# Optimization experiments

Hardware: AMD Instinct MI355X
Metric: run time of the kernel (lower is better)

Reference implementation:

```python
import jax, jax.numpy as jnp
import numpy as np

B, N, S, K = 16, 4096, 1024, 32
C_PTS = 64
MLP = [64, 64, 128]
EPS = 1e-5


def setup_inputs() -> dict:
    key = jax.random.key(0)
    ks = jax.random.split(key, 2 + len(MLP))
    inp = {
        "xyz": jax.random.normal(ks[0], (B, N, 3), jnp.float32),
        "points": jax.random.normal(ks[1], (B, N, C_PTS), jnp.float32),
    }
    last = 3 + C_PTS
    for i, o in enumerate(MLP):
        inp[f"w{i}"] = jax.random.normal(ks[2 + i], (o, last), jnp.float32) / np.sqrt(last).astype(np.float32)
        inp[f"b{i}"] = jnp.zeros((o,), jnp.float32)
        inp[f"gamma{i}"] = jnp.ones((o,), jnp.float32)
        inp[f"beta{i}"] = jnp.zeros((o,), jnp.float32)
        last = o
    return inp


def _farthest_point_sample(xyz, n_samples):
    # Sequential FPS; start index 0 (torch version uses a random start).
    b, n, _ = xyz.shape

    def step(carry, _):
        distance, farthest = carry  # [B,N], [B]
        centroid = jnp.take_along_axis(xyz, farthest[:, None, None], axis=1)  # [B,1,3]
        dist = jnp.sum((xyz - centroid) ** 2, axis=-1)  # [B,N]
        distance = jnp.minimum(distance, dist)
        new_far = jnp.argmax(distance, axis=-1).astype(jnp.int32)
        return (distance, new_far), farthest

    init = (jnp.full((b, n), 1e10, xyz.dtype), jnp.zeros((b,), jnp.int32))
    _, idxs = jax.lax.scan(step, init, None, length=n_samples)
    return idxs.T  # [B,S]


def _square_distance(src, dst):
    # ||src||^2 + ||dst||^2 - 2 src.dst  -> [B, S, N]
    return (jnp.sum(src ** 2, -1)[:, :, None]
            + jnp.sum(dst ** 2, -1)[:, None, :]
            - 2.0 * jnp.einsum('bsc,bnc->bsn', src, dst))


_gather = jax.vmap(lambda a, i: a[i])  # per-batch fancy gather


def _mlp_layer(x, w, bias, gamma, beta):
    # x: [B,S,K,Cin]; 1x1 conv == channel matmul, then training-mode BN over (B,S,K), then ReLU.
    y = jnp.einsum('bskc,oc->bsko', x, w) + bias
    mean = jnp.mean(y, axis=(0, 1, 2))
    var = jnp.mean((y - mean) ** 2, axis=(0, 1, 2))
    y = (y - mean) * jax.lax.rsqrt(var + EPS) * gamma + beta
    return jax.nn.relu(y)


def reference(xyz, points, w0, b0, gamma0, beta0, w1, b1, gamma1, beta1, w2, b2, gamma2, beta2):
    fps_idx = _farthest_point_sample(xyz, S)                   # [B,S]
    new_xyz = _gather(xyz, fps_idx)                            # [B,S,3]
    dists = _square_distance(new_xyz, xyz)                     # [B,S,N]
    nn_idx = jax.lax.top_k(-dists, K)[1]                       # [B,S,K]
    grouped_xyz = _gather(xyz, nn_idx)                         # [B,S,K,3]
    grouped_pts = _gather(points, nn_idx)                      # [B,S,K,C]
    feat = jnp.concatenate([grouped_xyz - new_xyz[:, :, None, :], grouped_pts], axis=-1)  # [B,S,K,3+C]
    x = _mlp_layer(feat, w0, b0, gamma0, beta0)
    x = _mlp_layer(x, w1, b1, gamma1, beta1)
    x = _mlp_layer(x, w2, b2, gamma2, beta2)
    new_points = jnp.max(x, axis=2)                            # [B,S,Cout]
    new_points = jnp.transpose(new_points, (0, 2, 1))          # [B,Cout,S] matches torch output
    return new_xyz, new_points
```

## Files before the change

kernel.cpp:

```cpp
#include <hip/hip_runtime.h>

#define B_ 16
#define N_ 4096
#define S_ 1024
#define K_ 32
#define NSLOT 128
#define CNT_F 524288.0f
#define RWS 524288

typedef unsigned short ushort_t;
typedef short short8 __attribute__((ext_vector_type(8)));
typedef float floatx4 __attribute__((ext_vector_type(4)));
union U4S8 { uint4 u; short8 v; };

__device__ __forceinline__ ushort_t f2bf(float f) {
  unsigned u = __float_as_uint(f);
  unsigned r = (u + 0x7fffu + ((u >> 16) & 1u)) >> 16;
  return (ushort_t)r;
}
__device__ __forceinline__ unsigned pkrne(float a, float b) {
  return (unsigned)f2bf(a) | ((unsigned)f2bf(b) << 16);
}
__device__ __forceinline__ unsigned pkhu(float a, float b) {
  return ((__float_as_uint(a) + 0x8000u) >> 16) |
         ((__float_as_uint(b) + 0x8000u) & 0xffff0000u);
}

__device__ __forceinline__ uint4 bn_relu_pack(uint4 xv, float4 sca, float4 scb,
                                              float4 sha, float4 shb) {
  float x0 = __uint_as_float(xv.x << 16);
  float x1 = __uint_as_float(xv.x & 0xffff0000u);
  float x2 = __uint_as_float(xv.y << 16);
  float x3 = __uint_as_float(xv.y & 0xffff0000u);
  float x4 = __uint_as_float(xv.z << 16);
  float x5 = __uint_as_float(xv.z & 0xffff0000u);
  float x6 = __uint_as_float(xv.w << 16);
  float x7 = __uint_as_float(xv.w & 0xffff0000u);
  x0 = fmaxf(fmaf(x0, sca.x, sha.x), 0.0f);
  x1 = fmaxf(fmaf(x1, sca.y, sha.y), 0.0f);
  x2 = fmaxf(fmaf(x2, sca.z, sha.z), 0.0f);
  x3 = fmaxf(fmaf(x3, sca.w, sha.w), 0.0f);
  x4 = fmaxf(fmaf(x4, scb.x, shb.x), 0.0f);
  x5 = fmaxf(fmaf(x5, scb.y, shb.y), 0.0f);
  x6 = fmaxf(fmaf(x6, scb.z, shb.z), 0.0f);
  x7 = fmaxf(fmaf(x7, scb.w, shb.w), 0.0f);
  return make_uint4(pkhu(x0, x1), pkhu(x2, x3), pkhu(x4, x5), pkhu(x6, x7));
}

#define FPS_T 256
#define FPS_P (N_ / FPS_T)
#define FPS_W (FPS_T / 64)

template <int CTRL>
__device__ __forceinline__ void dpp_max_u64(unsigned& hi, unsigned& lo) {
  unsigned h2 = (unsigned)__builtin_amdgcn_update_dpp(0, (int)hi, CTRL, 0xf, 0xf, true);
  unsigned l2 = (unsigned)__builtin_amdgcn_update_dpp(0, (int)lo, CTRL, 0xf, 0xf, true);
  bool take = (h2 > hi) || (h2 == hi && l2 > lo);
  hi = take ? h2 : hi;
  lo = take ? l2 : lo;
}

__global__ __launch_bounds__(256) void prep_all(
    const float* __restrict__ xyz, float* __restrict__ pt,
    const float* __restrict__ w0, const float* __restrict__ w1,
    const float* __restrict__ w2, ushort_t* __restrict__ wB0,
    ushort_t* __restrict__ wB1, ushort_t* __restrict__ wB2) {
  int i = blockIdx.x * 256 + threadIdx.x;
  float x = xyz[(size_t)i * 3 + 0];
  float y = xyz[(size_t)i * 3 + 1];
  float z = xyz[(size_t)i * 3 + 2];
  pt[i] = __fadd_rn(__fadd_rn(__fmul_rn(x, x), __fmul_rn(y, y)), __fmul_rn(z, z));
  if (i < 64 * 96) {
    int o = i / 96, c = i % 96;
    ushort_t v = 0;
    if (c < 64) v = f2bf(w0[o * 67 + 3 + c]);
    else if (c < 67) v = f2bf(w0[o * 67 + (c - 64)]);
    wB0[i] = v;
  }
  if (i < 64 * 64) wB1[i] = f2bf(w1[i]);
  if (i < 128 * 64) wB2[i] = f2bf(w2[i]);
}

#define SMEM_BYTES 56320
#define NBLK 512
#define NCONS_W ((NBLK - B_) * 4)

__global__ __launch_bounds__(256, 2) void fused_kernel(
    const float* __restrict__ xyz, const float* __restrict__ points,
    const float* __restrict__ ptn, const ushort_t* __restrict__ wB0,
    const float* __restrict__ bias0, int* __restrict__ pub,
    float* __restrict__ out_newxyz, ushort_t* __restrict__ y0,
    float* __restrict__ stats) {
  __shared__ __align__(16) char smem[SMEM_BYTES];
  int t = threadIdx.x;
  int w = t >> 6, l = t & 63;

  if (blockIdx.x < B_) {
    float* xyz_s = (float*)smem;
    int* idx_s = (int*)(smem + 49152);
    unsigned long long* keys_s = (unsigned long long*)(smem + 53248);
    int b = blockIdx.x;
    const float* xb = xyz + (size_t)b * N_ * 3;
    for (int i = t; i < N_ * 3; i += FPS_T) xyz_s[i] = xb[i];
    __syncthreads();
    float px[FPS_P], py[FPS_P], pz[FPS_P], dd[FPS_P];
#pragma unroll
    for (int j = 0; j < FPS_P; ++j) {
      int n = t + j * FPS_T;
      px[j] = xyz_s[n * 3 + 0];
      py[j] = xyz_s[n * 3 + 1];
      pz[j] = xyz_s[n * 3 + 2];
      dd[j] = 1e10f;
    }
    __builtin_amdgcn_s_setprio(3);
    int fi = 0;
#pragma unroll 1
    for (int s = 0; s < S_; ++s) {
      if (t == 0) {
        idx_s[s] = fi;
        __hip_atomic_store(&pub[(b << 10) + s], fi + 1, __ATOMIC_RELAXED,
                           __HIP_MEMORY_SCOPE_AGENT);
      }
      float cx = xyz_s[fi * 3 + 0], cy = xyz_s[fi * 3 + 1], cz = xyz_s[fi * 3 + 2];
      float bv = -1.0f;
      int bi = 0;
#pragma unroll
      for (int j = 0; j < FPS_P; ++j) {
        float dx = __fsub_rn(px[j], cx);
        float dy = __fsub_rn(py[j], cy);
        float dz = __fsub_rn(pz[j], cz);
        float d = __fadd_rn(__fadd_rn(__fmul_rn(dx, dx), __fmul_rn(dy, dy)),
                            __fmul_rn(dz, dz));
        d = fminf(dd[j], d);
        dd[j] = d;
        if (d > bv) { bv = d; bi = t + j * FPS_T; }
      }
      unsigned hi = __float_as_uint(bv);
      unsigned lo = (unsigned)(N_ - 1 - bi);
      dpp_max_u64<0x111>(hi, lo);
      dpp_max_u64<0x112>(hi, lo);
      dpp_max_u64<0x114>(hi, lo);
      dpp_max_u64<0x118>(hi, lo);
      dpp_max_u64<0x142>(hi, lo);
      dpp_max_u64<0x143>(hi, lo);
      unsigned whi = (unsigned)__builtin_amdgcn_readlane((int)hi, 63);
      unsigned wlo = (unsigned)__builtin_amdgcn_readlane((int)lo, 63);
      if ((t & 63) == 0)
        keys_s[(s & 1) * FPS_W + (t >> 6)] =
            ((unsigned long long)whi << 32) | wlo;
      __syncthreads();
      unsigned long long m = keys_s[(s & 1) * FPS_W + 0];
#pragma unroll
      for (int ww = 1; ww < FPS_W; ++ww) {
        unsigned long long k = keys_s[(s & 1) * FPS_W + ww];
        m = k > m ? k : m;
      }
      fi = (N_ - 1) - (int)(unsigned)(m & 0xFFFFFFFFULL);
    }
    __builtin_amdgcn_s_setprio(0);
    __syncthreads();
    for (int s = t; s < S_; s += FPS_T) {
      int i = idx_s[s];
      out_newxyz[((size_t)b * S_ + s) * 3 + 0] = xyz_s[i * 3 + 0];
      out_newxyz[((size_t)b * S_ + s) * 3 + 1] = xyz_s[i * 3 + 1];
      out_newxyz[((size_t)b * S_ + s) * 3 + 2] = xyz_s[i * 3 + 2];
    }
    return;
  }

  int n16 = l & 15, quad = l >> 4;
  U4S8 bf0[4][3];
  float b0v[4], ssum[4], ssq[4];
#pragma unroll
  for (int nt = 0; nt < 4; ++nt) {
#pragma unroll
    for (int kc = 0; kc < 3; ++kc)
      bf0[nt][kc].u = *reinterpret_cast<const uint4*>(
          wB0 + (size_t)(nt * 16 + n16) * 96 + kc * 32 + quad * 8);
    b0v[nt] = bias0[nt * 16 + n16];
    ssum[nt] = 0.0f;
    ssq[nt] = 0.0f;
  }
  float* ltw = (float*)(smem + w * (16 * 68 * 4));
  int wid = (blockIdx.x - B_) * 4 + w;

#pragma unroll 1
  for (int r = wid; r < B_ * S_; r += NCONS_W) {
    int b = r & 15, s = r >> 4;
    int bs = (b << 10) + s;
    int pv = 0;
    if (l == 0) {
      int tries = 0;
      while ((pv = __hip_atomic_load(&pub[bs], __ATOMIC_RELAXED,
                                     __HIP_MEMORY_SCOPE_AGENT)) == 0) {
        __builtin_amdgcn_s_sleep(32);
        if (++tries > 65536) break;
      }
    }
    pv = __shfl(pv, 0);
    int ci = pv - 1;
    if (ci < 0) ci = 0;
    const float* xb = xyz + (size_t)b * N_ * 3;
    const float* pnb = ptn + (size_t)b * N_;
    float sx = xb[ci * 3 + 0], sy = xb[ci * 3 + 1], sz = xb[ci * 3 + 2];
    float nxn = pnb[ci];

    unsigned u[64];
#pragma unroll
    for (int j = 0; j < 64; ++j) {
      int nn = j * 64 + l;
      float x = xb[nn * 3 + 0], y = xb[nn * 3 + 1], z = xb[nn * 3 + 2];
      float e = __fadd_rn(__fadd_rn(__fmul_rn(sx, x), __fmul_rn(sy, y)),
                          __fmul_rn(sz, z));
      float d = __fadd_rn(__fadd_rn(nxn, pnb[nn]), __fmul_rn(-2.0f, e));
      int sb = __float_as_int(d);
      u[j] = (sb < 0) ? ~((unsigned)sb) : (((unsigned)sb) | 0x80000000u);
    }
    unsigned keep = 0;
#pragma unroll 1
    for (int p = 0; p < K_; ++p) {
      unsigned gv[8], gj_[8];
#pragma unroll
      for (int g = 0; g < 8; ++g) {
        unsigned bv = u[g * 8];
        unsigned bj = (unsigned)(g * 8);
#pragma unroll
        for (int j2 = 1; j2 < 8; ++j2) {
          unsigned uu = u[g * 8 + j2];
          bool tk = uu < bv;
          bv = tk ? uu : bv;
          bj = tk ? (unsigned)(g * 8 + j2) : bj;
        }
        gv[g] = bv;
        gj_[g] = bj;
      }
#pragma unroll
      for (int st = 4; st >= 1; st >>= 1)
#pragma unroll
        for (int i2 = 0; i2 < 4; ++i2) {
          if (i2 < st) {
            bool tk = gv[i2 + st] < gv[i2];
            gv[i2] = tk ? gv[i2 + st] : gv[i2];
            gj_[i2] = tk ? gj_[i2 + st] : gj_[i2];
          }
        }
      unsigned hi = ~gv[0];
      unsigned lo = ~(gj_[0] * 64u + (unsigned)l);
      dpp_max_u64<0x111>(hi, lo);
      dpp_max_u64<0x112>(hi, lo);
      dpp_max_u64<0x114>(hi, lo);
      dpp_max_u64<0x118>(hi, lo);
      dpp_max_u64<0x142>(hi, lo);
      dpp_max_u64<0x143>(hi, lo);
      unsigned wlo = (unsigned)__builtin_amdgcn_readlane((int)lo, 63);
      unsigned gn = ~wlo;
      if (l == p) keep = gn;
      if ((gn & 63u) == (unsigned)l) {
        int gj = (int)(gn >> 6);
#pragma unroll
        for (int j = 0; j < 64; ++j)
          if (j == gj) u[j] = 0xFFFFFFFFu;
      }
    }

#pragma unroll 1
    for (int t2 = 0; t2 < 2; ++t2) {
      int rb = bs * 32 + t2 * 16;
      int idxr = __shfl((int)keep, t2 * 16 + n16);
      const float* pbase = points + (size_t)b * N_ * 64 + (size_t)idxr * 64;
      U4S8 af[3];
#pragma unroll
      for (int kc = 0; kc < 2; ++kc) {
        float4 va = *reinterpret_cast<const float4*>(pbase + kc * 32 + quad * 8);
        float4 vb = *reinterpret_cast<const float4*>(pbase + kc * 32 + quad * 8 + 4);
        af[kc].u = make_uint4(pkrne(va.x, va.y), pkrne(va.z, va.w),
                              pkrne(vb.x, vb.y), pkrne(vb.z, vb.w));
      }
      if (quad == 0) {
        const float* xb3 = xb + (size_t)idxr * 3;
        float dx = __fsub_rn(xb3[0], sx);
        float dy = __fsub_rn(xb3[1], sy);
        float dz = __fsub_rn(xb3[2], sz);
        af[2].u = make_uint4(pkrne(dx, dy), (unsigned)f2bf(dz), 0u, 0u);
      } else {
        af[2].u = make_uint4(0u, 0u, 0u, 0u);
      }
      floatx4 acc[4];
#pragma unroll
      for (int nt = 0; nt < 4; ++nt) acc[nt] = floatx4{0.f, 0.f, 0.f, 0.f};
#pragma unroll
      for (int kc = 0; kc < 3; ++kc)
#pragma unroll
        for (int nt = 0; nt < 4; ++nt)
          acc[nt] = __builtin_amdgcn_mfma_f32_16x16x32_bf16(
              af[kc].v, bf0[nt][kc].v, acc[nt], 0, 0, 0);
#pragma unroll
      for (int nt = 0; nt < 4; ++nt)
#pragma unroll
        for (int rI = 0; rI < 4; ++rI) {
          float ys = acc[nt][rI] + b0v[nt];
          ssum[nt] += ys;
          ssq[nt] = fmaf(ys, ys, ssq[nt]);
          ltw[(quad * 4 + rI) * 68 + nt * 16 + n16] = ys;
        }
      const float* lrow = ltw + n16 * 68 + quad * 16;
      float4 va = *reinterpret_cast<const float4*>(lrow);
      float4 vb = *reinterpret_cast<const float4*>(lrow + 4);
      float4 vc = *reinterpret_cast<const float4*>(lrow + 8);
      float4 vd = *reinterpret_cast<const float4*>(lrow + 12);
      ushort_t* yo = y0 + (size_t)(rb + n16) * 64 + quad * 16;
      *reinterpret_cast<uint4*>(yo) =
          make_uint4(pkhu(va.x, va.y), pkhu(va.z, va.w), pkhu(vb.x, vb.y), pkhu(vb.z, vb.w));
      *reinterpret_cast<uint4*>(yo + 8) =
          make_uint4(pkhu(vc.x, vc.y), pkhu(vc.z, vc.w), pkhu(vd.x, vd.y), pkhu(vd.z, vd.w));
    }
  }

  float* stp = stats + (size_t)(wid & (NSLOT - 1)) * 64 * 2;
#pragma unroll
  for (int nt = 0; nt < 4; ++nt) {
    float s = ssum[nt], q = ssq[nt];
    s += __shfl_down(s, 16); q += __shfl_down(q, 16);
    s += __shfl_down(s, 32); q += __shfl_down(q, 32);
    if (l < 16) {
      atomicAdd(&stp[(size_t)(nt * 16 + l) * 2 + 0], s);
      atomicAdd(&stp[(size_t)(nt * 16 + l) * 2 + 1], q);
    }
  }
}

__global__ __launch_bounds__(256) void gemm1_mfma(
    const ushort_t* __restrict__ y0, const float* __restrict__ bnp,
    const ushort_t* __restrict__ wB1, const float* __restrict__ bias1,
    ushort_t* __restrict__ y1, float* __restrict__ stats) {
  __shared__ __align__(16) float lt[4][16 * 68];
  int t = threadIdx.x;
  int w = t >> 6, l = t & 63;
  int n = l & 15, quad = l >> 4;
  U4S8 bf[4][2];
#pragma unroll
  for (int nt = 0; nt < 4; ++nt)
#pragma unroll
    for (int kc = 0; kc < 2; ++kc)
      bf[nt][kc].u = *reinterpret_cast<const uint4*>(
          wB1 + (size_t)(nt * 16 + n) * 64 + kc * 32 + quad * 8);
  float4 scA[2], scB[2], shA[2], shB[2];
#pragma unroll
  for (int kc = 0; kc < 2; ++kc) {
    int cb = kc * 32 + quad * 8;
    scA[kc] = *reinterpret_cast<const float4*>(&bnp[cb]);
    scB[kc] = *reinterpret_cast<const float4*>(&bnp[cb + 4]);
    shA[kc] = *reinterpret_cast<const float4*>(&bnp[64 + cb]);
    shB[kc] = *reinterpret_cast<const float4*>(&bnp[64 + cb + 4]);
  }
  float b1v[4], ssum[4], ssq[4];
#pragma unroll
  for (int nt = 0; nt < 4; ++nt) {
    b1v[nt] = bias1[nt * 16 + n];
    ssum[nt] = 0.0f;
    ssq[nt] = 0.0f;
  }
  int rowbase0 = blockIdx.x * 1024 + w * 256;
  float* ltw = lt[w];
#pragma unroll 1
  for (int tile = 0; tile < 16; ++tile) {
    int rb = rowbase0 + tile * 16;
    U4S8 af[2];
#pragma unroll
    for (int kc = 0; kc < 2; ++kc) {
      uint4 xv = *reinterpret_cast<const uint4*>(
          y0 + (size_t)(rb + n) * 64 + kc * 32 + quad * 8);
      af[kc].u = bn_relu_pack(xv, scA[kc], scB[kc], shA[kc], shB[kc]);
    }
    floatx4 acc[4];
#pragma unroll
    for (int nt = 0; nt < 4; ++nt) acc[nt] = floatx4{0.f, 0.f, 0.f, 0.f};
#pragma unroll
    for (int kc = 0; kc < 2; ++kc)
#pragma unroll
      for (int nt = 0; nt < 4; ++nt)
        acc[nt] = __builtin_amdgcn_mfma_f32_16x16x32_bf16(
            af[kc].v, bf[nt][kc].v, acc[nt], 0, 0, 0);
#pragma unroll
    for (int nt = 0; nt < 4; ++nt)
#pragma unroll
      for (int rI = 0; rI < 4; ++rI) {
        float ys = acc[nt][rI] + b1v[nt];
        ssum[nt] += ys;
        ssq[nt] = fmaf(ys, ys, ssq[nt]);
        ltw[(quad * 4 + rI) * 68 + nt * 16 + n] = ys;
      }
    const float* lrow = ltw + n * 68 + quad * 16;
    float4 va = *reinterpret_cast<const float4*>(lrow);
    float4 vb = *reinterpret_cast<const float4*>(lrow + 4);
    float4 vc = *reinterpret_cast<const float4*>(lrow + 8);
    float4 vd = *reinterpret_cast<const float4*>(lrow + 12);
    ushort_t* yo = y1 + (size_t)(rb + n) * 64 + quad * 16;
    *reinterpret_cast<uint4*>(yo) =
        make_uint4(pkhu(va.x, va.y), pkhu(va.z, va.w), pkhu(vb.x, vb.y), pkhu(vb.z, vb.w));
    *reinterpret_cast<uint4*>(yo + 8) =
        make_uint4(pkhu(vc.x, vc.y), pkhu(vc.z, vc.w), pkhu(vd.x, vd.y), pkhu(vd.z, vd.w));
  }
  float* stp = stats + (size_t)((blockIdx.x * 4 + w) & (NSLOT - 1)) * 64 * 2;
#pragma unroll
  for (int nt = 0; nt < 4; ++nt) {
    float s = ssum[nt], q = ssq[nt];
    s += __shfl_down(s, 16); q += __shfl_down(q, 16);
    s += __shfl_down(s, 32); q += __shfl_down(q, 32);
    if (l < 16) {
      atomicAdd(&stp[(size_t)(nt * 16 + l) * 2 + 0], s);
      atomicAdd(&stp[(size_t)(nt * 16 + l) * 2 + 1], q);
    }
  }
}

__global__ __launch_bounds__(256) void gemm2_mfma(
    const ushort_t* __restrict__ y1, const float* __restrict__ bnp,
    const ushort_t* __restrict__ wB2, const float* __restrict__ bias2,
    float* __restrict__ stats, float* __restrict__ maxY, float* __restrict__ minY) {
  int t = threadIdx.x;
  int w = t >> 6, l = t & 63;
  int n = l & 15, quad = l >> 4;
  U4S8 bf[8][2];
#pragma unroll
  for (int nt = 0; nt < 8; ++nt)
#pragma unroll
    for (int kc = 0; kc < 2; ++kc)
      bf[nt][kc].u = *reinterpret_cast<const uint4*>(
          wB2 + (size_t)(nt * 16 + n) * 64 + kc * 32 + quad * 8);
  float4 scA[2], scB[2], shA[2], shB[2];
#pragma unroll
  for (int kc = 0; kc < 2; ++kc) {
    int cb = kc * 32 + quad * 8;
    scA[kc] = *reinterpret_cast<const float4*>(&bnp[128 + cb]);
    scB[kc] = *reinterpret_cast<const float4*>(&bnp[128 + cb + 4]);
    shA[kc] = *reinterpret_cast<const float4*>(&bnp[192 + cb]);
    shB[kc] = *reinterpret_cast<const float4*>(&bnp[192 + cb + 4]);
  }
  float b2v[8], ssum[8], ssq[8], mxv[8], mnv[8];
#pragma unroll
  for (int nt = 0; nt < 8; ++nt) {
    b2v[nt] = bias2[nt * 16 + n];
    ssum[nt] = 0.0f;
    ssq[nt] = 0.0f;
    mxv[nt] = -3.4e38f;
    mnv[nt] = 3.4e38f;
  }
  int rowbase0 = blockIdx.x * 1024 + w * 256;
#pragma unroll 1
  for (int tile = 0; tile < 16; ++tile) {
    int rb = rowbase0 + tile * 16;
    U4S8 af[2];
#pragma unroll
    for (int kc = 0; kc < 2; ++kc) {
      uint4 xv = *reinterpret_cast<const uint4*>(
          y1 + (size_t)(rb + n) * 64 + kc * 32 + quad * 8);
      af[kc].u = bn_relu_pack(xv, scA[kc], scB[kc], shA[kc], shB[kc]);
    }
    floatx4 acc[8];
#pragma unroll
    for (int nt = 0; nt < 8; ++nt) acc[nt] = floatx4{0.f, 0.f, 0.f, 0.f};
#pragma unroll
    for (int kc = 0; kc < 2; ++kc)
#pragma unroll
      for (int nt = 0; nt < 8; ++nt)
        acc[nt] = __builtin_amdgcn_mfma_f32_16x16x32_bf16(
            af[kc].v, bf[nt][kc].v, acc[nt], 0, 0, 0);
#pragma unroll
    for (int nt = 0; nt < 8; ++nt)
#pragma unroll
      for (int rI = 0; rI < 4; ++rI) {
        float ya = acc[nt][rI] + b2v[nt];
        ssum[nt] += ya;
        ssq[nt] = fmaf(ya, ya, ssq[nt]);
        mxv[nt] = fmaxf(mxv[nt], ya);
        mnv[nt] = fminf(mnv[nt], ya);
      }
    if (tile & 1) {
      int sidx = (rowbase0 >> 5) + (tile >> 1);
#pragma unroll
      for (int nt = 0; nt < 8; ++nt) {
        float mx = mxv[nt], mn = mnv[nt];
        mx = fmaxf(mx, __shfl_down(mx, 16));
        mn = fminf(mn, __shfl_down(mn, 16));
        mx = fmaxf(mx, __shfl_down(mx, 32));
        mn = fminf(mn, __shfl_down(mn, 32));
        if (l < 16) {
          maxY[(size_t)sidx * 128 + nt * 16 + l] = mx;
          minY[(size_t)sidx * 128 + nt * 16 + l] = mn;
        }
        mxv[nt] = -3.4e38f;
        mnv[nt] = 3.4e38f;
      }
    }
  }
  float* stp = stats + (size_t)((blockIdx.x * 4 + w) & (NSLOT - 1)) * 128 * 2;
#pragma unroll
  for (int nt = 0; nt < 8; ++nt) {
    float s = ssum[nt], q = ssq[nt];
    s += __shfl_down(s, 16); q += __shfl_down(q, 16);
    s += __shfl_down(s, 32); q += __shfl_down(q, 32);
    if (l < 16) {
      atomicAdd(&stp[(size_t)(nt * 16 + l) * 2 + 0], s);
      atomicAdd(&stp[(size_t)(nt * 16 + l) * 2 + 1], q);
    }
  }
}

__global__ void bn_finalize(const float* __restrict__ st, int cout,
                            const float* __restrict__ gamma,
                            const float* __restrict__ beta,
                            float* __restrict__ scale, float* __restrict__ shift) {
  int o = threadIdx.x;
  if (o >= cout) return;
  float s = 0.0f, q = 0.0f;
  for (int i = 0; i < NSLOT; ++i) {
    s += st[((size_t)i * cout + o) * 2 + 0];
    q += st[((size_t)i * cout + o) * 2 + 1];
  }
  float mean = s * (1.0f / CNT_F);
  float var = q * (1.0f / CNT_F) - mean * mean;
  float sc = gamma[o] / sqrtf(var + 1e-5f);
  scale[o] = sc;
  shift[o] = beta[o] - mean * sc;
}

__global__ __launch_bounds__(256) void pool_kernel(
    const float* __restrict__ maxY, const float* __restrict__ minY,
    const float* __restrict__ bnp, float* __restrict__ out) {
  __shared__ float tile[128 * 65];
  int b = blockIdx.x >> 4;
  int sbase = (blockIdx.x & 15) * 64;
  int t = threadIdx.x;
#pragma unroll 4
  for (int i = 0; i < 32; ++i) {
    int e = i * 256 + t;
    int sl = e >> 7, o = e & 127;
    float sc = bnp[256 + o], sh = bnp[384 + o];
    size_t g = ((size_t)(b * S_ + sbase + sl)) * 128 + o;
    float v = (sc >= 0.0f) ? maxY[g] : minY[g];
    tile[o * 65 + sl] = fmaxf(fmaf(v, sc, sh), 0.0f);
  }
  __syncthreads();
  int sl = t & 63;
  for (int o2 = t >> 6; o2 < 128; o2 += 4) {
    out[((size_t)(b * 128 + o2)) * S_ + sbase + sl] = tile[o2 * 65 + sl];
  }
}

static inline size_t alup(size_t x) { return (x + 255) & ~(size_t)255; }

extern "C" void kernel_launch(void* const* d_in, const int* in_sizes, int n_in,
                              void* d_out, int out_size, void* d_ws, size_t ws_size,
                              hipStream_t stream) {
  (void)in_sizes; (void)n_in; (void)out_size;
  const float* xyz = (const float*)d_in[0];
  const float* points = (const float*)d_in[1];
  const float* w0 = (const float*)d_in[2];
  const float* b0 = (const float*)d_in[3];
  const float* g0 = (const float*)d_in[4];
  const float* be0 = (const float*)d_in[5];
  const float* w1 = (const float*)d_in[6];
  const float* b1 = (const float*)d_in[7];
  const float* g1 = (const float*)d_in[8];
  const float* be1 = (const float*)d_in[9];
  const float* w2 = (const float*)d_in[10];
  const float* b2 = (const float*)d_in[11];
  const float* g2 = (const float*)d_in[12];
  const float* be2 = (const float*)d_in[13];
  float* out_newxyz = (float*)d_out;
  float* out_newpts = out_newxyz + (size_t)B_ * S_ * 3;

  char* p = (char*)d_ws;
  int* pub = (int*)p;     p += alup((size_t)B_ * S_ * 4);
  float* ptn = (float*)p; p += alup((size_t)B_ * N_ * 4);
  float* st0 = (float*)p; p += (size_t)NSLOT * 64 * 2 * 4;
  float* st1 = (float*)p; p += (size_t)NSLOT * 64 * 2 * 4;
  float* st2 = (float*)p; p += (size_t)NSLOT * 128 * 2 * 4;
  float* bnp = (float*)p; p += alup(512 * 4);
  ushort_t* wB0 = (ushort_t*)p; p += alup(64 * 96 * 2);
  ushort_t* wB1 = (ushort_t*)p; p += alup(64 * 64 * 2);
  ushort_t* wB2 = (ushort_t*)p; p += alup(128 * 64 * 2);
  float* maxY = (float*)p; p += (size_t)B_ * S_ * 128 * 4;
  float* minY = (float*)p; p += (size_t)B_ * S_ * 128 * 4;
  ushort_t* y0 = (ushort_t*)p; p += (size_t)RWS * 64 * 2;
  ushort_t* y1 = (ushort_t*)p; p += (size_t)RWS * 64 * 2;
  if ((size_t)(p - (char*)d_ws) > ws_size) return;

  float* sc0 = bnp;       float* sh0 = bnp + 64;
  float* sc1 = bnp + 128; float* sh1 = bnp + 192;
  float* sc2 = bnp + 256; float* sh2 = bnp + 384;

  hipMemsetAsync(st0, 0, (size_t)NSLOT * (64 + 64 + 128) * 2 * 4, stream);
  hipMemsetAsync(pub, 0, (size_t)B_ * S_ * 4, stream);
  prep_all<<<256, 256, 0, stream>>>(xyz, ptn, w0, w1, w2, wB0, wB1, wB2);
  fused_kernel<<<NBLK, 256, 0, stream>>>(
      xyz, points, ptn, wB0, b0, pub, out_newxyz, y0, st0);
  bn_finalize<<<1, 128, 0, stream>>>(st0, 64, g0, be0, sc0, sh0);
  gemm1_mfma<<<RWS / 1024, 256, 0, stream>>>(y0, bnp, wB1, b1, y1, st1);
  bn_finalize<<<1, 128, 0, stream>>>(st1, 64, g1, be1, sc1, sh1);
  gemm2_mfma<<<RWS / 1024, 256, 0, stream>>>(y1, bnp, wB2, b2, st2, maxY, minY);
  bn_finalize<<<1, 128, 0, stream>>>(st2, 128, g2, be2, sc2, sh2);
  pool_kernel<<<B_ * (S_ / 64), 256, 0, stream>>>(maxY, minY, bnp, out_newpts);
}
```

Measured before the change: 910.3 us.

## Pack xyz and squared norm into float4 for kNN distance loads

The prep kernel now writes each point as a float4 (x, y, z, |p|^2) in place of a separate norm array. The kNN distance loop and the relative-xyz gather then read one 16-byte vector per point instead of four scalar loads. This is meant to cut load instruction count and uncoalesced strided access. Launch bounds for the fused kernel also drop from 2 to 1 blocks per CU, giving the compiler more registers for the 64-entry key array at the cost of occupancy.

```diff
diff --git a/kernel.cpp b/kernel.cpp
--- a/kernel.cpp
+++ b/kernel.cpp
@@ -61,7 +61,7 @@
 }
 
 __global__ __launch_bounds__(256) void prep_all(
-    const float* __restrict__ xyz, float* __restrict__ pt,
+    const float* __restrict__ xyz, float4* __restrict__ xyzw,
     const float* __restrict__ w0, const float* __restrict__ w1,
     const float* __restrict__ w2, ushort_t* __restrict__ wB0,
     ushort_t* __restrict__ wB1, ushort_t* __restrict__ wB2) {
@@ -69,7 +69,8 @@
   float x = xyz[(size_t)i * 3 + 0];
   float y = xyz[(size_t)i * 3 + 1];
   float z = xyz[(size_t)i * 3 + 2];
-  pt[i] = __fadd_rn(__fadd_rn(__fmul_rn(x, x), __fmul_rn(y, y)), __fmul_rn(z, z));
+  float nrm = __fadd_rn(__fadd_rn(__fmul_rn(x, x), __fmul_rn(y, y)), __fmul_rn(z, z));
+  xyzw[i] = make_float4(x, y, z, nrm);
   if (i < 64 * 96) {
     int o = i / 96, c = i % 96;
     ushort_t v = 0;
@@ -85,9 +86,9 @@
 #define NBLK 512
 #define NCONS_W ((NBLK - B_) * 4)
 
-__global__ __launch_bounds__(256, 2) void fused_kernel(
+__global__ __launch_bounds__(256, 1) void fused_kernel(
     const float* __restrict__ xyz, const float* __restrict__ points,
-    const float* __restrict__ ptn, const ushort_t* __restrict__ wB0,
+    const float4* __restrict__ xyzw, const ushort_t* __restrict__ wB0,
     const float* __restrict__ bias0, int* __restrict__ pub,
     float* __restrict__ out_newxyz, ushort_t* __restrict__ y0,
     float* __restrict__ stats) {
@@ -200,19 +201,19 @@
     pv = __shfl(pv, 0);
     int ci = pv - 1;
     if (ci < 0) ci = 0;
-    const float* xb = xyz + (size_t)b * N_ * 3;
-    const float* pnb = ptn + (size_t)b * N_;
-    float sx = xb[ci * 3 + 0], sy = xb[ci * 3 + 1], sz = xb[ci * 3 + 2];
-    float nxn = pnb[ci];
+    const float4* xw = xyzw + (size_t)b * N_;
+    float4 c4 = xw[ci];
+    float sx = c4.x, sy = c4.y, sz = c4.z;
+    float nxn = c4.w;
 
     unsigned u[64];
 #pragma unroll
     for (int j = 0; j < 64; ++j) {
       int nn = j * 64 + l;
-      float x = xb[nn * 3 + 0], y = xb[nn * 3 + 1], z = xb[nn * 3 + 2];
-      float e = __fadd_rn(__fadd_rn(__fmul_rn(sx, x), __fmul_rn(sy, y)),
-                          __fmul_rn(sz, z));
-      float d = __fadd_rn(__fadd_rn(nxn, pnb[nn]), __fmul_rn(-2.0f, e));
+      float4 v = xw[nn];
+      float e = __fadd_rn(__fadd_rn(__fmul_rn(sx, v.x), __fmul_rn(sy, v.y)),
+                          __fmul_rn(sz, v.z));
+      float d = __fadd_rn(__fadd_rn(nxn, v.w), __fmul_rn(-2.0f, e));
       int sb = __float_as_int(d);
       u[j] = (sb < 0) ? ~((unsigned)sb) : (((unsigned)sb) | 0x80000000u);
     }
@@ -277,10 +278,10 @@
                               pkrne(vb.x, vb.y), pkrne(vb.z, vb.w));
       }
       if (quad == 0) {
-        const float* xb3 = xb + (size_t)idxr * 3;
-        float dx = __fsub_rn(xb3[0], sx);
-        float dy = __fsub_rn(xb3[1], sy);
-        float dz = __fsub_rn(xb3[2], sz);
+        float4 p4 = xw[idxr];
+        float dx = __fsub_rn(p4.x, sx);
+        float dy = __fsub_rn(p4.y, sy);
+        float dz = __fsub_rn(p4.z, sz);
         af[2].u = make_uint4(pkrne(dx, dy), (unsigned)f2bf(dz), 0u, 0u);
       } else {
         af[2].u = make_uint4(0u, 0u, 0u, 0u);
@@ -572,12 +573,12 @@
   float* out_newpts = out_newxyz + (size_t)B_ * S_ * 3;
 
   char* p = (char*)d_ws;
-  int* pub = (int*)p;     p += alup((size_t)B_ * S_ * 4);
-  float* ptn = (float*)p; p += alup((size_t)B_ * N_ * 4);
-  float* st0 = (float*)p; p += (size_t)NSLOT * 64 * 2 * 4;
-  float* st1 = (float*)p; p += (size_t)NSLOT * 64 * 2 * 4;
-  float* st2 = (float*)p; p += (size_t)NSLOT * 128 * 2 * 4;
-  float* bnp = (float*)p; p += alup(512 * 4);
+  int* pub = (int*)p;      p += alup((size_t)B_ * S_ * 4);
+  float4* xyzw = (float4*)p; p += alup((size_t)B_ * N_ * 16);
+  float* st0 = (float*)p;  p += (size_t)NSLOT * 64 * 2 * 4;
+  float* st1 = (float*)p;  p += (size_t)NSLOT * 64 * 2 * 4;
+  float* st2 = (float*)p;  p += (size_t)NSLOT * 128 * 2 * 4;
+  float* bnp = (float*)p;  p += alup(512 * 4);
   ushort_t* wB0 = (ushort_t*)p; p += alup(64 * 96 * 2);
   ushort_t* wB1 = (ushort_t*)p; p += alup(64 * 64 * 2);
   ushort_t* wB2 = (ushort_t*)p; p += alup(128 * 64 * 2);
@@ -593,9 +594,9 @@
 
   hipMemsetAsync(st0, 0, (size_t)NSLOT * (64 + 64 + 128) * 2 * 4, stream);
   hipMemsetAsync(pub, 0, (size_t)B_ * S_ * 4, stream);
-  prep_all<<<256, 256, 0, stream>>>(xyz, ptn, w0, w1, w2, wB0, wB1, wB2);
+  prep_all<<<256, 256, 0, stream>>>(xyz, xyzw, w0, w1, w2, wB0, wB1, wB2);
   fused_kernel<<<NBLK, 256, 0, stream>>>(
-      xyz, points, ptn, wB0, b0, pub, out_newxyz, y0, st0);
+      xyz, points, xyzw, wB0, b0, pub, out_newxyz, y0, st0);
   bn_finalize<<<1, 128, 0, stream>>>(st0, 64, g0, be0, sc0, sh0);
   gemm1_mfma<<<RWS / 1024, 256, 0, stream>>>(y0, bnp, wB1, b1, y1, st1);
   bn_finalize<<<1, 128, 0, stream>>>(st1, 64, g1, be1, sc1, sh1);
```

Result: faster. 856.2 us (-5.9%).
